# Optimization experiments

Hardware: AMD Instinct MI355X
Metric: run time of the kernel (lower is better)

## Reference

```python
import jax, jax.numpy as jnp
import numpy as np

B, C, H, W = 8, 512, 64, 64


def setup_inputs() -> dict:
    key = jax.random.key(0)
    ks = jax.random.split(key, 8)
    return {
        "query": jax.random.normal(ks[0], (B, C, H, W), jnp.float32),
        "key": jax.random.normal(ks[1], (B, C, H, W), jnp.float32),
        "value": jax.random.normal(ks[2], (B, C, H, W), jnp.float32),
        "w1": jax.random.normal(ks[3], (4 * C, C), jnp.float32) * 0.02,
        "b1": jax.random.normal(ks[4], (4 * C,), jnp.float32) * 0.02,
        "w2": jax.random.normal(ks[5], (C, 4 * C), jnp.float32) * 0.02,
        "b2": jax.random.normal(ks[6], (C,), jnp.float32) * 0.02,
        "gamma": jax.random.normal(ks[7], (1,), jnp.float32),
    }


def reference(query, key, value, w1, b1, w2, b2, gamma):
    b, c, h, w = query.shape
    scale = c ** (-0.5)
    # flatten spatial dims: tokens n = h*w, channels c
    q = query.reshape(b, c, -1)   # [B,C,N]
    k = key.reshape(b, c, -1)     # [B,C,N]
    v = value.reshape(b, c, -1)   # [B,C,N]
    # attn[b,n,m] = softmax_m(q_n . k_m * scale)
    attn = jax.nn.softmax(jnp.einsum('bcn,bcm->bnm', q, k) * scale, axis=-1)
    out = jnp.einsum('bnm,bcm->bcn', attn, v).reshape(b, c, h, w)
    # 1x1-conv FFN: C -> 4C -> C with ReLU
    hdn = jax.nn.relu(jnp.einsum('bchw,dc->bdhw', out, w1) + b1[None, :, None, None])
    ffn = jnp.einsum('bdhw,cd->bchw', hdn, w2) + b2[None, :, None, None]
    return ffn * gamma + query
```

## Files before the change

### kernel.cpp

```cpp
#include <hip/hip_runtime.h>
#include <hip/hip_bf16.h>
#include <stdint.h>

#define BB 8
#define CC 512
#define NN 4096
#define QB 64
#define KB 64
#define D4 2048
#define NT (NN / KB)

typedef short bf8 __attribute__((ext_vector_type(8)));
typedef float f32x4 __attribute__((ext_vector_type(4)));

__device__ __forceinline__ uint16_t f2bf(float f) {
  uint32_t u = __builtin_bit_cast(uint32_t, f);
  u = (u + 0x7FFFu + ((u >> 16) & 1u)) >> 16;
  return (uint16_t)u;
}
__device__ __forceinline__ float bf2f(uint16_t u) {
  return __builtin_bit_cast(float, (uint32_t)u << 16);
}

__device__ __forceinline__ void gl_lds16(const void* g, void* l) {
  __builtin_amdgcn_global_load_lds((__attribute__((address_space(1))) void*)g,
                                   (__attribute__((address_space(3))) void*)l, 16, 0, 0);
}

__global__ __launch_bounds__(256) void transpose_cast_k(const float* __restrict__ src,
                                                        uint16_t* __restrict__ dst,
                                                        float scale) {
  __shared__ float tile[32][33];
  int b = blockIdx.z;
  int n0 = blockIdx.x * 32, c0 = blockIdx.y * 32;
  int tx = threadIdx.x & 31, ty = threadIdx.x >> 5;
  const float* s = src + ((size_t)b * CC + c0) * NN + n0;
#pragma unroll
  for (int i = 0; i < 4; i++) {
    int c = ty + i * 8;
    tile[tx][c] = s[(size_t)c * NN + tx];
  }
  __syncthreads();
  uint16_t* d = dst + ((size_t)b * NN + n0) * CC + c0;
#pragma unroll
  for (int i = 0; i < 4; i++) {
    int n = ty + i * 8;
    d[(size_t)n * CC + tx] = f2bf(tile[n][tx] * scale);
  }
}

__global__ __launch_bounds__(256) void cast_k(const float* __restrict__ in,
                                              uint16_t* __restrict__ out, int n) {
  int i = (blockIdx.x * 256 + threadIdx.x) * 4;
  if (i >= n) return;
  float4 v = *(const float4*)(in + i);
  ushort4 o;
  o.x = f2bf(v.x); o.y = f2bf(v.y); o.z = f2bf(v.z); o.w = f2bf(v.w);
  *(ushort4*)(out + i) = o;
}

__global__ __launch_bounds__(256) void vpack_k(const float* __restrict__ v,
                                               uint16_t* __restrict__ vp) {
  const int blk = blockIdx.x;
  const int w = blk & 7, mtb = blk >> 3;
  const int mt = mtb & (NT - 1), b = mtb >> 6;
  const int tid = threadIdx.x;
#pragma unroll
  for (int h = 0; h < 2; h++) {
    const int c = tid + h * 256;
    const int ks = c >> 8, rt = (c >> 6) & 3, l = c & 63;
    const int llo = l & 15, lhi = l >> 4;
    const float* src = v + ((size_t)b * CC + w * 64 + rt * 16 + llo) * NN + mt * 64 + ks * 32 + lhi * 8;
    const float4 f0 = *(const float4*)src;
    const float4 f1 = *(const float4*)(src + 4);
    ushort4 o0, o1;
    o0.x = f2bf(f0.x); o0.y = f2bf(f0.y); o0.z = f2bf(f0.z); o0.w = f2bf(f0.w);
    o1.x = f2bf(f1.x); o1.y = f2bf(f1.y); o1.z = f2bf(f1.z); o1.w = f2bf(f1.w);
    uint16_t* dst = vp + (size_t)blk * 4096 + ks * 2048 + rt * 512 + l * 8;
    *(ushort4*)dst = o0;
    *(ushort4*)(dst + 4) = o1;
  }
}

__global__ __launch_bounds__(512) __attribute__((amdgpu_waves_per_eu(2, 2))) void attn_ffn_k(
    const uint16_t* __restrict__ Qt, const uint16_t* __restrict__ Kt,
    const uint16_t* __restrict__ Vp, const uint16_t* __restrict__ W1b,
    const uint16_t* __restrict__ W2b, const float* __restrict__ b1v_,
    const float* __restrict__ b2, const float* __restrict__ gma,
    const float* __restrict__ qry, float* __restrict__ out) {
  __shared__ __attribute__((aligned(16))) uint16_t Ks[2][KB][CC];
  __shared__ __attribute__((aligned(16))) uint16_t SP[3][QB][72];
  __shared__ float rsc[3][QB];
  __shared__ float lst[QB];

  const int bid = blockIdx.x + gridDim.x * blockIdx.y;
  const int b = bid & 7;
  const int n0 = (bid >> 3) * QB;
  const int tid = threadIdx.x;
  const int lane = tid & 63, wid = tid >> 6;
  const int lhi = lane >> 4, llo = lane & 15;
  const int r7 = llo & 7;

  const int srt = wid >> 1;
  const int sct0 = (wid & 1) * 2;

  bf8 qf[16];
  {
    const uint16_t* qsrc = Qt + ((size_t)b * NN + n0 + srt * 16 + llo) * CC + lhi * 8;
#pragma unroll
    for (int kc = 0; kc < 16; kc++) qf[kc] = *(const bf8*)(qsrc + kc * 32);
  }

#pragma unroll
  for (int j = 0; j < 8; j++) {
    const int r = wid * 8 + j;
    gl_lds16(Kt + ((size_t)b * NN + r) * CC + ((lane ^ (r & 7)) << 3), &Ks[0][r][0]);
  }

  const f32x4 vzero = {0.f, 0.f, 0.f, 0.f};
  f32x4 acc[4][4];
#pragma unroll
  for (int i = 0; i < 4; i++)
#pragma unroll
    for (int j = 0; j < 4; j++) acc[i][j] = vzero;

  const uint16_t* vpw = Vp + (size_t)b * ((size_t)NT * 8 * 4096) + wid * 4096 + lane * 8;
  const int srow = tid >> 3, sj = tid & 7;
  float m_run = -__builtin_inff(), l_run = 0.f;
  bf8 av[2][4];

  auto QK = [&](int kbuf, int sb) {
    const uint16_t* k0row = &Ks[kbuf][sct0 * 16 + llo][0];
    const uint16_t* k1row = &Ks[kbuf][sct0 * 16 + 16 + llo][0];
    f32x4 s0 = vzero, s1 = vzero;
#pragma unroll
    for (int kc = 0; kc < 16; kc++) {
      const int g = ((kc * 4 + lhi) ^ r7) << 3;
      bf8 bk0 = *(const bf8*)(k0row + g);
      bf8 bk1 = *(const bf8*)(k1row + g);
      s0 = __builtin_amdgcn_mfma_f32_16x16x32_bf16(qf[kc], bk0, s0, 0, 0, 0);
      s1 = __builtin_amdgcn_mfma_f32_16x16x32_bf16(qf[kc], bk1, s1, 0, 0, 0);
    }
    const int n = srt * 16 + lhi * 4;
#pragma unroll
    for (int r = 0; r < 4; r++) {
      SP[sb][n + r][sct0 * 16 + llo] = f2bf(s0[r]);
      SP[sb][n + r][sct0 * 16 + 16 + llo] = f2bf(s1[r]);
    }
  };

  auto SOFTMAX = [&](int sb, bool last) {
    const bf8 sv8 = *(const bf8*)&SP[sb][srow][sj * 8];
    float sv[8];
#pragma unroll
    for (int k2 = 0; k2 < 8; k2++) sv[k2] = bf2f((uint16_t)sv8[k2]);
    float mx = fmaxf(fmaxf(fmaxf(sv[0], sv[1]), fmaxf(sv[2], sv[3])),
                     fmaxf(fmaxf(sv[4], sv[5]), fmaxf(sv[6], sv[7])));
    mx = fmaxf(mx, __shfl_xor(mx, 1, 8));
    mx = fmaxf(mx, __shfl_xor(mx, 2, 8));
    mx = fmaxf(mx, __shfl_xor(mx, 4, 8));
    const float nm = fmaxf(m_run, mx);
    const float rs = __expf(m_run - nm);
    float p[8], psum = 0.f;
#pragma unroll
    for (int k2 = 0; k2 < 8; k2++) {
      p[k2] = __expf(sv[k2] - nm);
      psum += p[k2];
    }
    bf8 pk;
#pragma unroll
    for (int k2 = 0; k2 < 8; k2++) pk[k2] = (short)f2bf(p[k2]);
    *(bf8*)&SP[sb][srow][sj * 8] = pk;
    psum += __shfl_xor(psum, 1, 8);
    psum += __shfl_xor(psum, 2, 8);
    psum += __shfl_xor(psum, 4, 8);
    l_run = l_run * rs + psum;
    m_run = nm;
    if (sj == 0) {
      rsc[sb][srow] = rs;
      if (last) lst[srow] = l_run;
    }
  };

  auto PV = [&](int sb) {
    float rsn[4];
#pragma unroll
    for (int nt = 0; nt < 4; nt++) rsn[nt] = rsc[sb][nt * 16 + llo];
#pragma unroll
    for (int rt = 0; rt < 4; rt++)
#pragma unroll
      for (int nt = 0; nt < 4; nt++) acc[rt][nt] *= rsn[nt];
#pragma unroll
    for (int ks = 0; ks < 2; ks++) {
      bf8 bp[4];
#pragma unroll
      for (int nt = 0; nt < 4; nt++)
        bp[nt] = *(const bf8*)&SP[sb][nt * 16 + llo][(ks * 4 + lhi) * 8];
#pragma unroll
      for (int rt = 0; rt < 4; rt++)
#pragma unroll
        for (int nt = 0; nt < 4; nt++)
          acc[rt][nt] = __builtin_amdgcn_mfma_f32_16x16x32_bf16(av[ks][rt], bp[nt], acc[rt][nt], 0, 0, 0);
    }
  };

  auto VLOAD = [&](int t) {
    const uint16_t* vt = vpw + (size_t)t * 32768;
#pragma unroll
    for (int ks = 0; ks < 2; ks++)
#pragma unroll
      for (int rt = 0; rt < 4; rt++)
        av[ks][rt] = *(const bf8*)(vt + ks * 2048 + rt * 512);
  };

  auto KDMA = [&](int t, int buf) {
#pragma unroll
    for (int j = 0; j < 8; j++) {
      const int r = wid * 8 + j;
      gl_lds16(Kt + ((size_t)b * NN + t * KB + r) * CC + ((lane ^ (r & 7)) << 3),
               &Ks[buf][r][0]);
    }
  };

  asm volatile("s_waitcnt vmcnt(0)" ::: "memory");
  __builtin_amdgcn_s_barrier();

  KDMA(1, 1);
  __builtin_amdgcn_s_setprio(1);
  QK(0, 0);
  __builtin_amdgcn_s_setprio(0);
  asm volatile("s_waitcnt vmcnt(0) lgkmcnt(0)" ::: "memory");
  __builtin_amdgcn_s_barrier();

  KDMA(2, 0);
  SOFTMAX(0, false);
  __builtin_amdgcn_s_setprio(1);
  QK(1, 1);
  __builtin_amdgcn_s_setprio(0);
  asm volatile("s_waitcnt vmcnt(0) lgkmcnt(0)" ::: "memory");
  __builtin_amdgcn_s_barrier();

  int sb0 = 2, sb1 = 1, sb2 = 0;
  for (int t = 2; t < NT; t++) {
    VLOAD(t - 2);
    if (t + 1 < NT) KDMA(t + 1, (t + 1) & 1);
    SOFTMAX(sb1, false);
    __builtin_amdgcn_s_setprio(1);
    PV(sb2);
    QK(t & 1, sb0);
    __builtin_amdgcn_s_setprio(0);
    asm volatile("s_waitcnt vmcnt(0) lgkmcnt(0)" ::: "memory");
    __builtin_amdgcn_s_barrier();
    const int tb = sb2; sb2 = sb1; sb1 = sb0; sb0 = tb;
  }

  VLOAD(NT - 2);
  SOFTMAX(sb1, true);
  __builtin_amdgcn_s_setprio(1);
  PV(sb2);
  __builtin_amdgcn_s_setprio(0);
  asm volatile("s_waitcnt vmcnt(0) lgkmcnt(0)" ::: "memory");
  __builtin_amdgcn_s_barrier();
  { const int tb = sb2; sb2 = sb1; sb1 = sb0; sb0 = tb; }

  VLOAD(NT - 1);
  __builtin_amdgcn_s_setprio(1);
  PV(sb2);
  __builtin_amdgcn_s_setprio(0);

  __syncthreads();

  float invl[4];
#pragma unroll
  for (int nt = 0; nt < 4; nt++) invl[nt] = 1.0f / lst[nt * 16 + llo];

  uint16_t(*Old)[CC] = (uint16_t(*)[CC]) & Ks[0][0][0];
#pragma unroll
  for (int rt = 0; rt < 4; rt++)
#pragma unroll
    for (int nt = 0; nt < 4; nt++) {
      ushort4 o4;
      o4.x = f2bf(acc[rt][nt][0] * invl[nt]);
      o4.y = f2bf(acc[rt][nt][1] * invl[nt]);
      o4.z = f2bf(acc[rt][nt][2] * invl[nt]);
      o4.w = f2bf(acc[rt][nt][3] * invl[nt]);
      const int gch = wid * 8 + rt * 2 + (lhi >> 1);
      *(ushort4*)(&Old[nt * 16 + llo][0] + ((gch ^ r7) << 3) + ((lhi & 1) << 2)) = o4;
    }

  uint16_t(*Hs)[CC] = (uint16_t(*)[CC]) & Ks[1][0][0];
  f32x4 facc[4][4];
#pragma unroll
  for (int i = 0; i < 4; i++)
#pragma unroll
    for (int j = 0; j < 4; j++) facc[i][j] = vzero;
  const float g = gma[0];
  const uint16_t* orow[4];
  const uint16_t* hrow[4];
#pragma unroll
  for (int nt = 0; nt < 4; nt++) {
    orow[nt] = &Old[nt * 16 + llo][0];
    hrow[nt] = &Hs[nt * 16 + llo][0];
  }

  for (int qtr = 0; qtr < 4; qtr++) {
    const int dq0 = qtr * 512;
    f32x4 hacc[4][4];
#pragma unroll
    for (int i = 0; i < 4; i++)
#pragma unroll
      for (int j = 0; j < 4; j++) hacc[i][j] = vzero;
    __syncthreads();
    __builtin_amdgcn_s_setprio(1);
#pragma unroll 2
    for (int kc8 = 0; kc8 < 64; kc8 += 4) {
      bf8 bo[4], aw[4];
      const int gof = ((kc8 + lhi) ^ r7) << 3;
#pragma unroll
      for (int nt = 0; nt < 4; nt++) bo[nt] = *(const bf8*)(orow[nt] + gof);
#pragma unroll
      for (int dt = 0; dt < 4; dt++) {
        const int d = dq0 + wid * 64 + dt * 16 + llo;
        aw[dt] = *(const bf8*)(W1b + (size_t)d * CC + (kc8 + lhi) * 8);
      }
#pragma unroll
      for (int dt = 0; dt < 4; dt++)
#pragma unroll
        for (int nt = 0; nt < 4; nt++)
          hacc[dt][nt] = __builtin_amdgcn_mfma_f32_16x16x32_bf16(aw[dt], bo[nt], hacc[dt][nt], 0, 0, 0);
    }
    __builtin_amdgcn_s_setprio(0);
#pragma unroll
    for (int dt = 0; dt < 4; dt++) {
      const int dg = dq0 + wid * 64 + dt * 16 + lhi * 4;
      const float4 b1v = *(const float4*)(b1v_ + dg);
#pragma unroll
      for (int nt = 0; nt < 4; nt++) {
        ushort4 h4;
        h4.x = f2bf(fmaxf(hacc[dt][nt][0] + b1v.x, 0.f));
        h4.y = f2bf(fmaxf(hacc[dt][nt][1] + b1v.y, 0.f));
        h4.z = f2bf(fmaxf(hacc[dt][nt][2] + b1v.z, 0.f));
        h4.w = f2bf(fmaxf(hacc[dt][nt][3] + b1v.w, 0.f));
        const int gch = wid * 8 + dt * 2 + (lhi >> 1);
        *(ushort4*)(&Hs[nt * 16 + llo][0] + ((gch ^ r7) << 3) + ((lhi & 1) << 2)) = h4;
      }
    }
    __syncthreads();
    __builtin_amdgcn_s_setprio(1);
#pragma unroll 2
    for (int kd8 = 0; kd8 < 64; kd8 += 4) {
      bf8 ah[4], bw[4];
      const int gof = ((kd8 + lhi) ^ r7) << 3;
#pragma unroll
      for (int nt = 0; nt < 4; nt++) ah[nt] = *(const bf8*)(hrow[nt] + gof);
#pragma unroll
      for (int ct = 0; ct < 4; ct++) {
        const int c = wid * 64 + ct * 16 + llo;
        bw[ct] = *(const bf8*)(W2b + (size_t)c * D4 + dq0 + (kd8 + lhi) * 8);
      }
#pragma unroll
      for (int nt = 0; nt < 4; nt++)
#pragma unroll
        for (int ct = 0; ct < 4; ct++)
          facc[nt][ct] = __builtin_amdgcn_mfma_f32_16x16x32_bf16(ah[nt], bw[ct], facc[nt][ct], 0, 0, 0);
    }
    __builtin_amdgcn_s_setprio(0);
  }

#pragma unroll
  for (int nt = 0; nt < 4; nt++) {
    const int n = n0 + nt * 16 + lhi * 4;
#pragma unroll
    for (int ct = 0; ct < 4; ct++) {
      const int c = wid * 64 + ct * 16 + llo;
      const float b2c = b2[c];
      const size_t off = ((size_t)b * CC + c) * NN + n;
      const float4 q4 = *(const float4*)(qry + off);
      float4 o4;
      o4.x = (facc[nt][ct][0] + b2c) * g + q4.x;
      o4.y = (facc[nt][ct][1] + b2c) * g + q4.y;
      o4.z = (facc[nt][ct][2] + b2c) * g + q4.z;
      o4.w = (facc[nt][ct][3] + b2c) * g + q4.w;
      *(float4*)(out + off) = o4;
    }
  }
}

extern "C" void kernel_launch(void* const* d_in, const int* in_sizes, int n_in,
                              void* d_out, int out_size, void* d_ws, size_t ws_size,
                              hipStream_t stream) {
  const float* q = (const float*)d_in[0];
  const float* k = (const float*)d_in[1];
  const float* v = (const float*)d_in[2];
  const float* w1 = (const float*)d_in[3];
  const float* b1 = (const float*)d_in[4];
  const float* w2 = (const float*)d_in[5];
  const float* b2 = (const float*)d_in[6];
  const float* gm = (const float*)d_in[7];
  float* out = (float*)d_out;

  uint16_t* Qt = (uint16_t*)d_ws;
  uint16_t* Kt = Qt + (size_t)BB * NN * CC;
  uint16_t* Vp = Kt + (size_t)BB * NN * CC;
  uint16_t* W1b = Vp + (size_t)BB * NN * CC;
  uint16_t* W2b = W1b + (size_t)D4 * CC;

  dim3 tgrid(NN / 32, CC / 32, BB);
  transpose_cast_k<<<tgrid, 256, 0, stream>>>(q, Qt, 0.044194173824159216f);
  transpose_cast_k<<<tgrid, 256, 0, stream>>>(k, Kt, 1.0f);
  vpack_k<<<BB * NT * 8, 256, 0, stream>>>(v, Vp);
  cast_k<<<(D4 * CC / 4 + 255) / 256, 256, 0, stream>>>(w1, W1b, D4 * CC);
  cast_k<<<(CC * D4 / 4 + 255) / 256, 256, 0, stream>>>(w2, W2b, CC * D4);
  attn_ffn_k<<<dim3(NN / QB, BB), 512, 0, stream>>>(Qt, Kt, Vp, W1b, W2b, b1, b2, gm, q, out);
}
```

Measured before the change: 708.0 us.

## Swizzle score tile in LDS and double-buffer FFN hidden slices

Applies an XOR swizzle to the score/probability tile in LDS so the QK writes, softmax accesses and PV reads avoid bank conflicts. The FFN stage now works on eight 256-wide hidden slices that alternate between two LDS buffers. The first GEMM for slice s runs alongside the second GEMM for slice s-1, which leaves one barrier per slice instead of two syncthreads per quarter. This gives more overlap and fewer barriers, but each W1 pass does less work per slice, and the manual waitcnt/barrier placement needs care.

```diff
diff --git a/kernel.cpp b/kernel.cpp
--- a/kernel.cpp
+++ b/kernel.cpp
@@ -126,6 +126,7 @@
 
   const uint16_t* vpw = Vp + (size_t)b * ((size_t)NT * 8 * 4096) + wid * 4096 + lane * 8;
   const int srow = tid >> 3, sj = tid & 7;
+  const int sgc = (sj ^ (srow & 7)) << 3;
   float m_run = -__builtin_inff(), l_run = 0.f;
   bf8 av[2][4];
 
@@ -141,16 +142,19 @@
       s0 = __builtin_amdgcn_mfma_f32_16x16x32_bf16(qf[kc], bk0, s0, 0, 0, 0);
       s1 = __builtin_amdgcn_mfma_f32_16x16x32_bf16(qf[kc], bk1, s1, 0, 0, 0);
     }
-    const int n = srt * 16 + lhi * 4;
+    const int nr = srt * 16 + lhi * 4;
+    const int gb = sct0 * 2 + (llo >> 3);
+    const int el = llo & 7;
 #pragma unroll
     for (int r = 0; r < 4; r++) {
-      SP[sb][n + r][sct0 * 16 + llo] = f2bf(s0[r]);
-      SP[sb][n + r][sct0 * 16 + 16 + llo] = f2bf(s1[r]);
+      const int row7 = (lhi * 4 + r) & 7;
+      SP[sb][nr + r][((gb ^ row7) << 3) + el] = f2bf(s0[r]);
+      SP[sb][nr + r][(((gb + 2) ^ row7) << 3) + el] = f2bf(s1[r]);
     }
   };
 
   auto SOFTMAX = [&](int sb, bool last) {
-    const bf8 sv8 = *(const bf8*)&SP[sb][srow][sj * 8];
+    const bf8 sv8 = *(const bf8*)&SP[sb][srow][sgc];
     float sv[8];
 #pragma unroll
     for (int k2 = 0; k2 < 8; k2++) sv[k2] = bf2f((uint16_t)sv8[k2]);
@@ -170,7 +174,7 @@
     bf8 pk;
 #pragma unroll
     for (int k2 = 0; k2 < 8; k2++) pk[k2] = (short)f2bf(p[k2]);
-    *(bf8*)&SP[sb][srow][sj * 8] = pk;
+    *(bf8*)&SP[sb][srow][sgc] = pk;
     psum += __shfl_xor(psum, 1, 8);
     psum += __shfl_xor(psum, 2, 8);
     psum += __shfl_xor(psum, 4, 8);
@@ -195,7 +199,7 @@
       bf8 bp[4];
 #pragma unroll
       for (int nt = 0; nt < 4; nt++)
-        bp[nt] = *(const bf8*)&SP[sb][nt * 16 + llo][(ks * 4 + lhi) * 8];
+        bp[nt] = *(const bf8*)&SP[sb][nt * 16 + llo][(((ks * 4 + lhi) ^ r7) << 3)];
 #pragma unroll
       for (int rt = 0; rt < 4; rt++)
 #pragma unroll
@@ -287,53 +291,50 @@
       const int gch = wid * 8 + rt * 2 + (lhi >> 1);
       *(ushort4*)(&Old[nt * 16 + llo][0] + ((gch ^ r7) << 3) + ((lhi & 1) << 2)) = o4;
     }
-
-  uint16_t(*Hs)[CC] = (uint16_t(*)[CC]) & Ks[1][0][0];
-  f32x4 facc[4][4];
-#pragma unroll
-  for (int i = 0; i < 4; i++)
-#pragma unroll
-    for (int j = 0; j < 4; j++) facc[i][j] = vzero;
+  asm volatile("s_waitcnt lgkmcnt(0)" ::: "memory");
+  __builtin_amdgcn_s_barrier();
+
+  uint16_t* Hb0 = &Ks[1][0][0];
+  uint16_t* Hb1 = &Ks[1][32][0];
   const float g = gma[0];
   const uint16_t* orow[4];
-  const uint16_t* hrow[4];
-#pragma unroll
-  for (int nt = 0; nt < 4; nt++) {
-    orow[nt] = &Old[nt * 16 + llo][0];
-    hrow[nt] = &Hs[nt * 16 + llo][0];
-  }
-
-  for (int qtr = 0; qtr < 4; qtr++) {
-    const int dq0 = qtr * 512;
-    f32x4 hacc[4][4];
-#pragma unroll
-    for (int i = 0; i < 4; i++)
+#pragma unroll
+  for (int nt = 0; nt < 4; nt++) orow[nt] = &Old[nt * 16 + llo][0];
+
+  f32x4 facc[4][4];
+#pragma unroll
+  for (int i = 0; i < 4; i++)
+#pragma unroll
+    for (int j = 0; j < 4; j++) facc[i][j] = vzero;
+
+  auto FG1 = [&](int sl) {
+    const int dq0 = sl * 256;
+    uint16_t* Hw = (sl & 1) ? Hb1 : Hb0;
+    f32x4 hacc[2][4];
+#pragma unroll
+    for (int i = 0; i < 2; i++)
 #pragma unroll
       for (int j = 0; j < 4; j++) hacc[i][j] = vzero;
-    __syncthreads();
     __builtin_amdgcn_s_setprio(1);
 #pragma unroll 2
     for (int kc8 = 0; kc8 < 64; kc8 += 4) {
-      bf8 bo[4], aw[4];
+      bf8 bo[4], aw[2];
       const int gof = ((kc8 + lhi) ^ r7) << 3;
 #pragma unroll
       for (int nt = 0; nt < 4; nt++) bo[nt] = *(const bf8*)(orow[nt] + gof);
 #pragma unroll
-      for (int dt = 0; dt < 4; dt++) {
-        const int d = dq0 + wid * 64 + dt * 16 + llo;
-        aw[dt] = *(const bf8*)(W1b + (size_t)d * CC + (kc8 + lhi) * 8);
-      }
-#pragma unroll
-      for (int dt = 0; dt < 4; dt++)
+      for (int dt = 0; dt < 2; dt++)
+        aw[dt] = *(const bf8*)(W1b + (size_t)(dq0 + wid * 32 + dt * 16 + llo) * CC + (kc8 + lhi) * 8);
+#pragma unroll
+      for (int dt = 0; dt < 2; dt++)
 #pragma unroll
         for (int nt = 0; nt < 4; nt++)
           hacc[dt][nt] = __builtin_amdgcn_mfma_f32_16x16x32_bf16(aw[dt], bo[nt], hacc[dt][nt], 0, 0, 0);
     }
     __builtin_amdgcn_s_setprio(0);
 #pragma unroll
-    for (int dt = 0; dt < 4; dt++) {
-      const int dg = dq0 + wid * 64 + dt * 16 + lhi * 4;
-      const float4 b1v = *(const float4*)(b1v_ + dg);
+    for (int dt = 0; dt < 2; dt++) {
+      const float4 b1v = *(const float4*)(b1v_ + dq0 + wid * 32 + dt * 16 + lhi * 4);
 #pragma unroll
       for (int nt = 0; nt < 4; nt++) {
         ushort4 h4;
@@ -341,23 +342,28 @@
         h4.y = f2bf(fmaxf(hacc[dt][nt][1] + b1v.y, 0.f));
         h4.z = f2bf(fmaxf(hacc[dt][nt][2] + b1v.z, 0.f));
         h4.w = f2bf(fmaxf(hacc[dt][nt][3] + b1v.w, 0.f));
-        const int gch = wid * 8 + dt * 2 + (lhi >> 1);
-        *(ushort4*)(&Hs[nt * 16 + llo][0] + ((gch ^ r7) << 3) + ((lhi & 1) << 2)) = h4;
+        const int row = nt * 16 + llo;
+        const int gch = wid * 4 + dt * 2 + (lhi >> 1);
+        *(ushort4*)(Hw + row * 256 + ((gch ^ r7) << 3) + ((lhi & 1) << 2)) = h4;
       }
     }
-    __syncthreads();
+  };
+
+  auto FG2 = [&](int sl) {
+    const int dq0 = sl * 256;
+    const uint16_t* Hr = (sl & 1) ? Hb1 : Hb0;
     __builtin_amdgcn_s_setprio(1);
 #pragma unroll 2
-    for (int kd8 = 0; kd8 < 64; kd8 += 4) {
+    for (int kd8 = 0; kd8 < 32; kd8 += 4) {
       bf8 ah[4], bw[4];
-      const int gof = ((kd8 + lhi) ^ r7) << 3;
-#pragma unroll
-      for (int nt = 0; nt < 4; nt++) ah[nt] = *(const bf8*)(hrow[nt] + gof);
-#pragma unroll
-      for (int ct = 0; ct < 4; ct++) {
-        const int c = wid * 64 + ct * 16 + llo;
-        bw[ct] = *(const bf8*)(W2b + (size_t)c * D4 + dq0 + (kd8 + lhi) * 8);
+#pragma unroll
+      for (int nt = 0; nt < 4; nt++) {
+        const int row = nt * 16 + llo;
+        ah[nt] = *(const bf8*)(Hr + row * 256 + (((kd8 + lhi) ^ r7) << 3));
       }
+#pragma unroll
+      for (int ct = 0; ct < 4; ct++)
+        bw[ct] = *(const bf8*)(W2b + (size_t)(wid * 64 + ct * 16 + llo) * D4 + dq0 + (kd8 + lhi) * 8);
 #pragma unroll
       for (int nt = 0; nt < 4; nt++)
 #pragma unroll
@@ -365,7 +371,18 @@
           facc[nt][ct] = __builtin_amdgcn_mfma_f32_16x16x32_bf16(ah[nt], bw[ct], facc[nt][ct], 0, 0, 0);
     }
     __builtin_amdgcn_s_setprio(0);
-  }
+  };
+
+  FG1(0);
+  asm volatile("s_waitcnt lgkmcnt(0)" ::: "memory");
+  __builtin_amdgcn_s_barrier();
+  for (int sl = 1; sl < 8; sl++) {
+    FG1(sl);
+    FG2(sl - 1);
+    asm volatile("s_waitcnt lgkmcnt(0)" ::: "memory");
+    __builtin_amdgcn_s_barrier();
+  }
+  FG2(7);
 
 #pragma unroll
   for (int nt = 0; nt < 4; nt++) {
```

Result: slower. 725.7 us (+2.5%).
